# Kernel tuning notes

Hardware: AMD Instinct MI355X
Metric: run time of the kernel (lower is better)

## Reference

```python
import jax, jax.numpy as jnp
import numpy as np

N = 50000          # nodes
E = 600000         # edges
D_IN = 256         # input_feat_dim
H1 = 128           # hidden_dim1
H2 = 64            # hidden_dim2
DK = 64            # trs_depth (total key/value depth)
HEADS = 2


def setup_inputs() -> dict:
    key = jax.random.key(0)
    ks = jax.random.split(key, 12)
    inp = {
        "ns_emb": jax.random.normal(ks[0], (N, D_IN), dtype=jnp.float32),
        "edge_rows": jax.random.randint(ks[1], (E,), 0, N, dtype=jnp.int32),
        "edge_cols": jax.random.randint(ks[2], (E,), 0, N, dtype=jnp.int32),
        "edge_vals": jax.random.uniform(ks[3], (E,), dtype=jnp.float32),
        "condition": jax.random.normal(ks[4], (1, 128, H1), dtype=jnp.float32),
        # GCN linear weights (bias=False), stored [in, out]
        "W_hidden": jax.random.normal(ks[5], (D_IN, H1), dtype=jnp.float32) / np.sqrt(D_IN),
        "W_mu": jax.random.normal(ks[6], (H1, H2), dtype=jnp.float32) / np.sqrt(H1),
        "W_var": jax.random.normal(ks[7], (H1, H2), dtype=jnp.float32) / np.sqrt(H1),
        # MultiHeadAttention (bias-free) projections
        "Wq": jax.random.normal(ks[8], (H1, DK), dtype=jnp.float32) / np.sqrt(H1),
        "Wk": jax.random.normal(ks[9], (H1, DK), dtype=jnp.float32) / np.sqrt(H1),
        "Wv": jax.random.normal(ks[10], (H1, DK), dtype=jnp.float32) / np.sqrt(H1),
        "Wo": jax.random.normal(ks[11], (DK, H1), dtype=jnp.float32) / np.sqrt(DK),
    }
    return inp


def _spmm(rows, cols, vals, x):
    # sparse [N,N] @ x  via gather + segment-sum over COO edges
    gathered = vals[:, None] * x[cols]            # [E, d]
    return jax.ops.segment_sum(gathered, rows, num_segments=N)


def _gcn(x, W, rows, cols, vals):
    # dropout is identity in eval mode
    support = jax.nn.leaky_relu(x @ W)            # [N, out]
    out = _spmm(rows, cols, vals, support)        # [N, out]
    return jax.nn.leaky_relu(out)


def _mha(q, kv, Wq, Wk, Wv, Wo):
    # MoEL-style MultiHeadAttention, bias-free, no mask/dropout
    B, Lq, _ = q.shape
    Lk = kv.shape[1]
    dk = DK // HEADS
    Q = (q @ Wq).reshape(B, Lq, HEADS, dk).transpose(0, 2, 1, 3) * (dk ** -0.5)
    K = (kv @ Wk).reshape(B, Lk, HEADS, dk).transpose(0, 2, 1, 3)
    V = (kv @ Wv).reshape(B, Lk, HEADS, dk).transpose(0, 2, 1, 3)
    logits = jnp.einsum("bhqd,bhkd->bhqk", Q, K)
    w = jax.nn.softmax(logits, axis=-1)
    ctx = jnp.einsum("bhqk,bhkd->bhqd", w, V)
    ctx = ctx.transpose(0, 2, 1, 3).reshape(B, Lq, DK)
    return ctx @ Wo, w


def reference(ns_emb, edge_rows, edge_cols, edge_vals, condition,
              W_hidden, W_mu, W_var, Wq, Wk, Wv, Wo):
    hidden = _gcn(ns_emb, W_hidden, edge_rows, edge_cols, edge_vals)   # [N, H1]
    attended, _ = _mha(hidden[None], condition, Wq, Wk, Wv, Wo)        # [1, N, H1]
    h = attended[0]
    mu = _gcn(h, W_mu, edge_rows, edge_cols, edge_vals)                # [N, H2]
    var = _gcn(h, W_var, edge_rows, edge_cols, edge_vals)              # [N, H2]
    return mu, var
```

## Files before the change

kernel.cpp:

```cpp
#include <hip/hip_runtime.h>
#include <hip/hip_bf16.h>
#include <cstdint>


typedef __attribute__((ext_vector_type(8))) short short8;
typedef __attribute__((ext_vector_type(4))) float f32x4;
typedef __attribute__((ext_vector_type(4))) unsigned short ushort4_t;

__device__ __forceinline__ unsigned short f2bf(float f) {
    unsigned int u = __builtin_bit_cast(unsigned int, f);
    u += 0x7fffu + ((u >> 16) & 1u);
    return (unsigned short)(u >> 16);
}
__device__ __forceinline__ float bf2f(unsigned short v) {
    return __builtin_bit_cast(float, (unsigned int)v << 16);
}


__global__ void hist_kernel(const int* __restrict__ rows, int* __restrict__ cnt, int E) {
    int i = blockIdx.x * blockDim.x + threadIdx.x;
    if (i < E) atomicAdd(&cnt[rows[i]], 1);
}

__global__ void scan1_kernel(const int* __restrict__ cnt, int* __restrict__ excl,
                             int* __restrict__ bsum, int N) {
    __shared__ int sh[256];
    int t = threadIdx.x;
    int i = blockIdx.x * 256 + t;
    int v = (i < N) ? cnt[i] : 0;
    sh[t] = v;
    __syncthreads();
    for (int off = 1; off < 256; off <<= 1) {
        int x = (t >= off) ? sh[t - off] : 0;
        __syncthreads();
        sh[t] += x;
        __syncthreads();
    }
    if (i < N) excl[i] = sh[t] - v;
    if (t == 255) bsum[blockIdx.x] = sh[255];
}

__global__ void scan23_kernel(const int* __restrict__ excl, const int* __restrict__ bsum,
                              int* __restrict__ row_start, int* __restrict__ cursor,
                              int nb, int N, int E) {
    __shared__ int sh[256];
    int t = threadIdx.x;
    int v = (t < nb) ? bsum[t] : 0;
    sh[t] = v;
    __syncthreads();
    for (int off = 1; off < 256; off <<= 1) {
        int x = (t >= off) ? sh[t - off] : 0;
        __syncthreads();
        sh[t] += x;
        __syncthreads();
    }
    int boff = (blockIdx.x > 0) ? sh[blockIdx.x - 1] : 0;
    int i = blockIdx.x * 256 + t;
    if (i < N) {
        int w = excl[i] + boff;
        row_start[i] = w;
        cursor[i] = w;
    }
    if (i == 0) row_start[N] = E;
}

__global__ void scatter_kernel(const int* __restrict__ rows, const int* __restrict__ colsIn,
                               const float* __restrict__ valsIn, int* __restrict__ cursor,
                               int2* __restrict__ pack, int E) {
    int i = blockIdx.x * blockDim.x + threadIdx.x;
    if (i < E) {
        int r = rows[i];
        int p = atomicAdd(&cursor[r], 1);
        pack[p] = make_int2(colsIn[i], __float_as_int(valsIn[i]));
    }
}


__global__ __launch_bounds__(256) void prep_kv_kernel(
    const float* __restrict__ Wh, const float* __restrict__ Wq,
    const float* __restrict__ cond,
    const float* __restrict__ Wk, const float* __restrict__ Wv,
    const float* __restrict__ Wo, const float* __restrict__ Wmu,
    const float* __restrict__ Wvar,
    unsigned short* __restrict__ WhT, unsigned short* __restrict__ WqT,
    unsigned short* __restrict__ Ktt, unsigned short* __restrict__ Vt,
    unsigned short* __restrict__ WomT)
{
    const int t = threadIdx.x;
    const int bid = blockIdx.x;
    if (bid < 160) {
        int idx = bid * 256 + t;
        if (idx < 32768) {
            int n = idx & 127, k = idx >> 7;
            WhT[n * 256 + k] = f2bf(Wh[k * 128 + n]);
        } else {
            int i = idx - 32768, n = i & 63, k = i >> 6;
            WqT[n * 128 + k] = f2bf(Wq[k * 64 + n]);
        }
    } else if (bid < 224) {
        int b2 = bid - 160;
        __shared__ float c[2][128];
        c[t >> 7][t & 127] = cond[b2 * 256 + t];
        __syncthreads();
        int j = b2 * 2 + (t >> 7);
        int tl = t & 127;
        const float* W = (tl < 64) ? Wk : Wv;
        int col = tl & 63;
        float acc = 0.f;
#pragma unroll 8
        for (int k = 0; k < 128; ++k) acc = fmaf(c[t >> 7][k], W[k * 64 + col], acc);
        int h = col >> 5, d = col & 31;
        if (tl < 64) Ktt[((size_t)h * 128 + j) * 32 + d] = f2bf(acc * 0.17677669529663687f);
        else         Vt[((size_t)h * 32 + d) * 128 + j] = f2bf(acc);
    } else {
        int wb = bid - 224;
        __shared__ float WoTl[128 * 65];
#pragma unroll
        for (int i = 0; i < 32; ++i) {
            int idx = t + 256 * i;
            int d = idx >> 7, k = idx & 127;
            WoTl[k * 65 + d] = Wo[idx];
        }
        __syncthreads();
        int o = wb * 256 + t;
        int d = o & 63, n = o >> 6;
        const float* W = (n < 64) ? Wmu : Wvar;
        int j = n & 63;
        float acc = 0.f;
#pragma unroll 8
        for (int k = 0; k < 128; ++k) acc = fmaf(WoTl[k * 65 + d], W[k * 64 + j], acc);
        WomT[n * 64 + d] = f2bf(acc);
    }
}


__global__ __launch_bounds__(256) void gcn1_gemm(
    const float* __restrict__ A, const unsigned short* __restrict__ BT,
    unsigned short* __restrict__ C, int M)
{
    __shared__ unsigned short As[128][72];
    __shared__ unsigned short Bs[128][72];

    const int tid = threadIdx.x;
    const int lane = tid & 63, wave = tid >> 6;
    const int wm = wave & 1, wn = wave >> 1;
    const int quad = lane >> 4, l16 = lane & 15;
    const int r0 = blockIdx.x * 128;

    f32x4 acc[4][4];
#pragma unroll
    for (int mt = 0; mt < 4; ++mt)
#pragma unroll
        for (int nt = 0; nt < 4; ++nt)
#pragma unroll
            for (int r = 0; r < 4; ++r) acc[mt][nt][r] = 0.f;

    for (int kc = 0; kc < 256; kc += 64) {
#pragma unroll
        for (int i = 0; i < 8; ++i) {
            int f = tid + 256 * i;
            int row = f >> 4, kq = (f & 15) << 2;
            int gr = r0 + row;
            if (gr >= M) gr = M - 1;
            float4 v = *reinterpret_cast<const float4*>(&A[(size_t)gr * 256 + kc + kq]);
            unsigned int lo, hi;
            asm("v_cvt_pk_bf16_f32 %0, %1, %2" : "=v"(lo) : "v"(v.x), "v"(v.y));
            asm("v_cvt_pk_bf16_f32 %0, %1, %2" : "=v"(hi) : "v"(v.z), "v"(v.w));
            *reinterpret_cast<uint2*>(&As[row][kq]) = make_uint2(lo, hi);
        }
#pragma unroll
        for (int i = 0; i < 4; ++i) {
            int f = tid + 256 * i;
            int n = f >> 3, k8 = (f & 7) << 3;
            *reinterpret_cast<short8*>(&Bs[n][k8]) =
                *reinterpret_cast<const short8*>(&BT[(size_t)n * 256 + kc + k8]);
        }
        __syncthreads();

#pragma unroll
        for (int ks = 0; ks < 2; ++ks) {
            const int koff = ks * 32 + quad * 8;
            short8 a[4], b[4];
#pragma unroll
            for (int mt = 0; mt < 4; ++mt)
                a[mt] = *reinterpret_cast<const short8*>(&As[wm * 64 + mt * 16 + l16][koff]);
#pragma unroll
            for (int nt = 0; nt < 4; ++nt)
                b[nt] = *reinterpret_cast<const short8*>(&Bs[wn * 64 + nt * 16 + l16][koff]);
#pragma unroll
            for (int mt = 0; mt < 4; ++mt)
#pragma unroll
                for (int nt = 0; nt < 4; ++nt)
                    acc[mt][nt] = __builtin_amdgcn_mfma_f32_16x16x32_bf16(
                        a[mt], b[nt], acc[mt][nt], 0, 0, 0);
        }
        __syncthreads();
    }

#pragma unroll
    for (int mt = 0; mt < 4; ++mt)
#pragma unroll
        for (int nt = 0; nt < 4; ++nt) {
            int gc = wn * 64 + nt * 16 + l16;
#pragma unroll
            for (int r = 0; r < 4; ++r) {
                int gr = r0 + wm * 64 + mt * 16 + quad * 4 + r;
                if (gr < M) {
                    float v = acc[mt][nt][r];
                    v = v > 0.f ? v : 0.01f * v;
                    C[(size_t)gr * 128 + gc] = f2bf(v);
                }
            }
        }
}


__global__ __launch_bounds__(256) void attn_muvar_kernel(
    const unsigned short* __restrict__ support1,
    const int* __restrict__ row_start,
    const int2* __restrict__ pack,
    const unsigned short* __restrict__ WqT,
    const unsigned short* __restrict__ Ktt,
    const unsigned short* __restrict__ Vt,
    const unsigned short* __restrict__ WomT,
    unsigned short* __restrict__ muvar,
    int M)
{
    __shared__ unsigned short Ap[128 * 136];
    __shared__ unsigned short Bp[10240];
    __shared__ unsigned short Cp[128 * 72];
    __shared__ float redm[2][128];
    __shared__ float reds[2][128];

    const int tid = threadIdx.x;
    const int lane = tid & 63, wave = tid >> 6;
    const int wm = wave & 1, wn = wave >> 1;
    const int quad = lane >> 4, l16 = lane & 15;
    const int r0 = blockIdx.x * 128;

#pragma unroll
    for (int i = 0; i < 4; ++i) {
        int f = tid + 256 * i;
        int n = f >> 4, k8 = (f & 15) << 3;
        *reinterpret_cast<short8*>(&Bp[n * 136 + k8]) =
            *reinterpret_cast<const short8*>(&WqT[(size_t)n * 128 + k8]);
    }

    {
        const int fo = lane * 2;
        const int base = r0 + wave * 32;
        const bool fast = (base + 32 <= M);
        int bnds = 0;
        if (fast && lane <= 32) bnds = row_start[base + lane];

        for (int it = 0; it < 32; ++it) {
            int row = wave * 32 + it;
            int s, e;
            if (fast) {
                s = __shfl(bnds, it, 64);
                e = __shfl(bnds, it + 1, 64);
            } else {
                int gr = r0 + row;
                if (gr >= M) gr = M - 1;
                s = __builtin_amdgcn_readfirstlane(row_start[gr]);
                e = __builtin_amdgcn_readfirstlane(row_start[gr + 1]);
            }

            float ax[8], ay[8];
#pragma unroll
            for (int k = 0; k < 8; ++k) { ax[k] = 0.f; ay[k] = 0.f; }

            int i = s;
            for (; i + 8 <= e; i += 8) {
                int2 p[8];
                unsigned int x[8];
#pragma unroll
                for (int k = 0; k < 8; ++k) p[k] = pack[i + k];
#pragma unroll
                for (int k = 0; k < 8; ++k)
                    x[k] = *reinterpret_cast<const unsigned int*>(&support1[(size_t)p[k].x * 128 + fo]);
#pragma unroll
                for (int k = 0; k < 8; ++k) {
                    float v = __int_as_float(p[k].y);
                    ax[k] = fmaf(v, bf2f((unsigned short)x[k]), ax[k]);
                    ay[k] = fmaf(v, bf2f((unsigned short)(x[k] >> 16)), ay[k]);
                }
            }
            if (i < e) {
                int2 p[8];
                unsigned int x[8];
#pragma unroll
                for (int k = 0; k < 8; ++k) {
                    int idx = i + k;
                    p[k] = pack[idx < e ? idx : e - 1];
                }
#pragma unroll
                for (int k = 0; k < 8; ++k)
                    x[k] = *reinterpret_cast<const unsigned int*>(&support1[(size_t)p[k].x * 128 + fo]);
#pragma unroll
                for (int k = 0; k < 8; ++k) {
                    float v = (i + k < e) ? __int_as_float(p[k].y) : 0.f;
                    ax[k] = fmaf(v, bf2f((unsigned short)x[k]), ax[k]);
                    ay[k] = fmaf(v, bf2f((unsigned short)(x[k] >> 16)), ay[k]);
                }
            }

            float ox = ((ax[0] + ax[1]) + (ax[2] + ax[3])) + ((ax[4] + ax[5]) + (ax[6] + ax[7]));
            float oy = ((ay[0] + ay[1]) + (ay[2] + ay[3])) + ((ay[4] + ay[5]) + (ay[6] + ay[7]));
            ox = ox > 0.f ? ox : 0.01f * ox;
            oy = oy > 0.f ? oy : 0.01f * oy;
            unsigned int w = (unsigned int)f2bf(ox) | ((unsigned int)f2bf(oy) << 16);
            *reinterpret_cast<unsigned int*>(&Ap[row * 136 + fo]) = w;
        }
    }
    __syncthreads();

    {
        f32x4 accq[4][2];
#pragma unroll
        for (int mt = 0; mt < 4; ++mt)
#pragma unroll
            for (int nt = 0; nt < 2; ++nt)
#pragma unroll
                for (int r = 0; r < 4; ++r) accq[mt][nt][r] = 0.f;
#pragma unroll
        for (int ks = 0; ks < 4; ++ks) {
            const int koff = ks * 32 + quad * 8;
            short8 a[4], b[2];
#pragma unroll
            for (int mt = 0; mt < 4; ++mt)
                a[mt] = *reinterpret_cast<const short8*>(&Ap[(wm * 64 + mt * 16 + l16) * 136 + koff]);
#pragma unroll
            for (int nt = 0; nt < 2; ++nt)
                b[nt] = *reinterpret_cast<const short8*>(&Bp[(wn * 32 + nt * 16 + l16) * 136 + koff]);
#pragma unroll
            for (int mt = 0; mt < 4; ++mt)
#pragma unroll
                for (int nt = 0; nt < 2; ++nt)
                    accq[mt][nt] = __builtin_amdgcn_mfma_f32_16x16x32_bf16(
                        a[mt], b[nt], accq[mt][nt], 0, 0, 0);
        }
#pragma unroll
        for (int mt = 0; mt < 4; ++mt)
#pragma unroll
            for (int nt = 0; nt < 2; ++nt) {
                int col = wn * 32 + nt * 16 + l16;
#pragma unroll
                for (int r = 0; r < 4; ++r) {
                    int row = wm * 64 + mt * 16 + quad * 4 + r;
                    Cp[row * 72 + col] = f2bf(accq[mt][nt][r]);
                }
            }
    }
    __syncthreads();

    for (int h = 0; h < 2; ++h) {
#pragma unroll
        for (int i = 0; i < 2; ++i) {
            int f = tid + 256 * i;
            int key = f >> 2, d8 = (f & 3) << 3;
            *reinterpret_cast<short8*>(&Bp[key * 40 + d8]) =
                *reinterpret_cast<const short8*>(&Ktt[((size_t)h * 128 + key) * 32 + d8]);
        }
#pragma unroll
        for (int i = 0; i < 2; ++i) {
            int f = tid + 256 * i;
            int d = f >> 4, k8 = (f & 15) << 3;
            *reinterpret_cast<short8*>(&Bp[5120 + d * 136 + k8]) =
                *reinterpret_cast<const short8*>(&Vt[((size_t)h * 32 + d) * 128 + k8]);
        }
        __syncthreads();

        f32x4 accl[4][4];
        {
            short8 a[4], b[4];
#pragma unroll
            for (int mt = 0; mt < 4; ++mt)
                a[mt] = *reinterpret_cast<const short8*>(&Cp[(wm * 64 + mt * 16 + l16) * 72 + h * 32 + quad * 8]);
#pragma unroll
            for (int nt = 0; nt < 4; ++nt)
                b[nt] = *reinterpret_cast<const short8*>(&Bp[(wn * 64 + nt * 16 + l16) * 40 + quad * 8]);
#pragma unroll
            for (int mt = 0; mt < 4; ++mt)
#pragma unroll
                for (int nt = 0; nt < 4; ++nt) {
                    f32x4 z; z[0] = 0.f; z[1] = 0.f; z[2] = 0.f; z[3] = 0.f;
                    accl[mt][nt] = __builtin_amdgcn_mfma_f32_16x16x32_bf16(a[mt], b[nt], z, 0, 0, 0);
                }
        }

#pragma unroll
        for (int mt = 0; mt < 4; ++mt)
#pragma unroll
            for (int r = 0; r < 4; ++r) {
                float mx = fmaxf(fmaxf(accl[mt][0][r], accl[mt][1][r]),
                                 fmaxf(accl[mt][2][r], accl[mt][3][r]));
#pragma unroll
                for (int off = 1; off < 16; off <<= 1)
                    mx = fmaxf(mx, __shfl_xor(mx, off, 64));
                if (l16 == 0) redm[wn][wm * 64 + mt * 16 + quad * 4 + r] = mx;
            }
        __syncthreads();
#pragma unroll
        for (int mt = 0; mt < 4; ++mt)
#pragma unroll
            for (int r = 0; r < 4; ++r) {
                int lr = wm * 64 + mt * 16 + quad * 4 + r;
                float fm = fmaxf(redm[0][lr], redm[1][lr]);
                float s = 0.f;
#pragma unroll
                for (int nt = 0; nt < 4; ++nt) {
                    float e = __expf(accl[mt][nt][r] - fm);
                    accl[mt][nt][r] = e;
                    s += e;
                }
#pragma unroll
                for (int off = 1; off < 16; off <<= 1)
                    s += __shfl_xor(s, off, 64);
                if (l16 == 0) reds[wn][lr] = s;
            }
        __syncthreads();
#pragma unroll
        for (int mt = 0; mt < 4; ++mt)
#pragma unroll
            for (int r = 0; r < 4; ++r) {
                int lr = wm * 64 + mt * 16 + quad * 4 + r;
                float inv = 1.0f / (reds[0][lr] + reds[1][lr]);
#pragma unroll
                for (int nt = 0; nt < 4; ++nt)
                    Ap[lr * 136 + wn * 64 + nt * 16 + l16] = f2bf(accl[mt][nt][r] * inv);
            }
        __syncthreads();

        {
            f32x4 accc[4];
#pragma unroll
            for (int mt = 0; mt < 4; ++mt)
#pragma unroll
                for (int r = 0; r < 4; ++r) accc[mt][r] = 0.f;
#pragma unroll
            for (int ks = 0; ks < 4; ++ks) {
                const int koff = ks * 32 + quad * 8;
                short8 a[4];
#pragma unroll
                for (int mt = 0; mt < 4; ++mt)
                    a[mt] = *reinterpret_cast<const short8*>(&Ap[(wm * 64 + mt * 16 + l16) * 136 + koff]);
                short8 bb = *reinterpret_cast<const short8*>(&Bp[5120 + (wn * 16 + l16) * 136 + koff]);
#pragma unroll
                for (int mt = 0; mt < 4; ++mt)
                    accc[mt] = __builtin_amdgcn_mfma_f32_16x16x32_bf16(a[mt], bb, accc[mt], 0, 0, 0);
            }
#pragma unroll
            for (int mt = 0; mt < 4; ++mt)
#pragma unroll
                for (int r = 0; r < 4; ++r) {
                    int row = wm * 64 + mt * 16 + quad * 4 + r;
                    Cp[row * 72 + h * 32 + wn * 16 + l16] = f2bf(accc[mt][r]);
                }
        }
        __syncthreads();
    }

#pragma unroll
    for (int i = 0; i < 4; ++i) {
        int f = tid + 256 * i;
        int n = f >> 3, k8 = (f & 7) << 3;
        *reinterpret_cast<short8*>(&Bp[n * 72 + k8]) =
            *reinterpret_cast<const short8*>(&WomT[(size_t)n * 64 + k8]);
    }
    __syncthreads();
    {
        f32x4 accf[4][4];
#pragma unroll
        for (int mt = 0; mt < 4; ++mt)
#pragma unroll
            for (int nt = 0; nt < 4; ++nt)
#pragma unroll
                for (int r = 0; r < 4; ++r) accf[mt][nt][r] = 0.f;
#pragma unroll
        for (int ks = 0; ks < 2; ++ks) {
            const int koff = ks * 32 + quad * 8;
            short8 a[4], b[4];
#pragma unroll
            for (int mt = 0; mt < 4; ++mt)
                a[mt] = *reinterpret_cast<const short8*>(&Cp[(wm * 64 + mt * 16 + l16) * 72 + koff]);
#pragma unroll
            for (int nt = 0; nt < 4; ++nt)
                b[nt] = *reinterpret_cast<const short8*>(&Bp[(wn * 64 + nt * 16 + l16) * 72 + koff]);
#pragma unroll
            for (int mt = 0; mt < 4; ++mt)
#pragma unroll
                for (int nt = 0; nt < 4; ++nt)
                    accf[mt][nt] = __builtin_amdgcn_mfma_f32_16x16x32_bf16(
                        a[mt], b[nt], accf[mt][nt], 0, 0, 0);
        }
#pragma unroll
        for (int mt = 0; mt < 4; ++mt)
#pragma unroll
            for (int nt = 0; nt < 4; ++nt) {
                int gc = wn * 64 + nt * 16 + l16;
#pragma unroll
                for (int r = 0; r < 4; ++r) {
                    int gr = r0 + wm * 64 + mt * 16 + quad * 4 + r;
                    if (gr < M) {
                        float v = accf[mt][nt][r];
                        v = v > 0.f ? v : 0.01f * v;
                        muvar[(size_t)gr * 128 + gc] = f2bf(v);
                    }
                }
            }
    }
}


template<bool SPLIT, typename OT>
__global__ __launch_bounds__(256) void spmm_kernel(
    const int* __restrict__ row_start, const int2* __restrict__ pack,
    const unsigned short* __restrict__ X,
    OT* __restrict__ out0, OT* __restrict__ out1, int N)
{
    const int wave = threadIdx.x >> 6, lane = threadIdx.x & 63;
    const int r = blockIdx.x * 4 + wave;
    if (r >= N) return;
    int s = __builtin_amdgcn_readfirstlane(row_start[r]);
    int e = __builtin_amdgcn_readfirstlane(row_start[r + 1]);
    const int fo = lane * 2;

    float ax[8], ay[8];
#pragma unroll
    for (int k = 0; k < 8; ++k) { ax[k] = 0.f; ay[k] = 0.f; }

    int i = s;
    for (; i + 8 <= e; i += 8) {
        int2 p[8];
        unsigned int x[8];
#pragma unroll
        for (int k = 0; k < 8; ++k) p[k] = pack[i + k];
#pragma unroll
        for (int k = 0; k < 8; ++k)
            x[k] = *reinterpret_cast<const unsigned int*>(&X[(size_t)p[k].x * 128 + fo]);
#pragma unroll
        for (int k = 0; k < 8; ++k) {
            float v = __int_as_float(p[k].y);
            ax[k] = fmaf(v, bf2f((unsigned short)x[k]), ax[k]);
            ay[k] = fmaf(v, bf2f((unsigned short)(x[k] >> 16)), ay[k]);
        }
    }
    if (i < e) {
        int2 p[8];
        unsigned int x[8];
#pragma unroll
        for (int k = 0; k < 8; ++k) {
            int idx = i + k;
            p[k] = pack[idx < e ? idx : e - 1];
        }
#pragma unroll
        for (int k = 0; k < 8; ++k)
            x[k] = *reinterpret_cast<const unsigned int*>(&X[(size_t)p[k].x * 128 + fo]);
#pragma unroll
        for (int k = 0; k < 8; ++k) {
            float v = (i + k < e) ? __int_as_float(p[k].y) : 0.f;
            ax[k] = fmaf(v, bf2f((unsigned short)x[k]), ax[k]);
            ay[k] = fmaf(v, bf2f((unsigned short)(x[k] >> 16)), ay[k]);
        }
    }

    float ox = ((ax[0] + ax[1]) + (ax[2] + ax[3])) + ((ax[4] + ax[5]) + (ax[6] + ax[7]));
    float oy = ((ay[0] + ay[1]) + (ay[2] + ay[3])) + ((ay[4] + ay[5]) + (ay[6] + ay[7]));
    ox = ox > 0.f ? ox : 0.01f * ox;
    oy = oy > 0.f ? oy : 0.01f * oy;

    if constexpr (!SPLIT) {
        unsigned int w = (unsigned int)f2bf(ox) | ((unsigned int)f2bf(oy) << 16);
        *reinterpret_cast<unsigned int*>(&out0[(size_t)r * 128 + fo]) = w;
    } else {
        if (lane < 32) {
            *reinterpret_cast<float2*>(&out0[(size_t)r * 64 + fo]) = make_float2(ox, oy);
        } else {
            *reinterpret_cast<float2*>(&out1[(size_t)r * 64 + (fo - 64)]) = make_float2(ox, oy);
        }
    }
}


extern "C" void kernel_launch(void* const* d_in, const int* in_sizes, int n_in,
                              void* d_out, int out_size, void* d_ws, size_t ws_size,
                              hipStream_t stream)
{
    const float* ns_emb   = (const float*)d_in[0];
    const int*   erows    = (const int*)d_in[1];
    const int*   ecols    = (const int*)d_in[2];
    const float* evals    = (const float*)d_in[3];
    const float* cond     = (const float*)d_in[4];
    const float* W_hidden = (const float*)d_in[5];
    const float* W_mu     = (const float*)d_in[6];
    const float* W_var    = (const float*)d_in[7];
    const float* Wq       = (const float*)d_in[8];
    const float* Wk       = (const float*)d_in[9];
    const float* Wv       = (const float*)d_in[10];
    const float* Wo       = (const float*)d_in[11];

    const int N = in_sizes[0] / 256;
    const int E = in_sizes[1];

    typedef unsigned short bf16;
    uint8_t* p = (uint8_t*)d_ws;
    auto alloc = [&](size_t bytes) {
        uint8_t* r = p;
        p += (bytes + 255) & ~(size_t)255;
        return r;
    };
    bf16* support1 = (bf16*)alloc(sizeof(bf16) * (size_t)N * 128);
    bf16* muvarb   = (bf16*)alloc(sizeof(bf16) * (size_t)N * 128);
    bf16* Ktt      = (bf16*)alloc(sizeof(bf16) * 2 * 128 * 32);
    bf16* Vt       = (bf16*)alloc(sizeof(bf16) * 2 * 32 * 128);
    bf16* WhT      = (bf16*)alloc(sizeof(bf16) * 128 * 256);
    bf16* WqT      = (bf16*)alloc(sizeof(bf16) * 64 * 128);
    bf16* WomT     = (bf16*)alloc(sizeof(bf16) * 128 * 64);
    int*  cnt      = (int*)alloc(sizeof(int) * N);
    int*  excl     = (int*)alloc(sizeof(int) * N);
    int*  bsum     = (int*)alloc(sizeof(int) * 256);
    int*  row_start= (int*)alloc(sizeof(int) * (N + 1));
    int*  cursor   = (int*)alloc(sizeof(int) * N);
    int2* pack     = (int2*)alloc(sizeof(int2) * E);

    hipMemsetAsync(cnt, 0, sizeof(int) * N, stream);
    hist_kernel<<<(E + 255) / 256, 256, 0, stream>>>(erows, cnt, E);
    int nb = (N + 255) / 256;
    scan1_kernel<<<nb, 256, 0, stream>>>(cnt, excl, bsum, N);
    scan23_kernel<<<nb, 256, 0, stream>>>(excl, bsum, row_start, cursor, nb, N, E);
    scatter_kernel<<<(E + 255) / 256, 256, 0, stream>>>(erows, ecols, evals, cursor, pack, E);

    prep_kv_kernel<<<256, 256, 0, stream>>>(W_hidden, Wq, cond, Wk, Wv,
                                            Wo, W_mu, W_var,
                                            WhT, WqT, Ktt, Vt, WomT);

    const int mb = (N + 127) / 128;
    const int sblocks = (N + 3) / 4;

    gcn1_gemm<<<mb, 256, 0, stream>>>(ns_emb, WhT, support1, N);

    attn_muvar_kernel<<<mb, 256, 0, stream>>>(support1, row_start, pack,
                                              WqT, Ktt, Vt, WomT, muvarb, N);

    float* out = (float*)d_out;
    spmm_kernel<true, float><<<sblocks, 256, 0, stream>>>(
        row_start, pack, muvarb, out, out + (size_t)N * 64, N);
}
```

Measured before the change: 301.4 us.

## Split first SpMM out of attention kernel and halve attention tile rows

Moves the first-layer sparse aggregation out of the fused attention kernel into a separate wave-per-row spmm_kernel that writes a bf16 hidden buffer. The attention kernel then just loads the dense hidden tile and works on 64-row tiles instead of 128, which cuts LDS use and doubles the block count. The fused version had each wave walk 32 rows one after another with poor parallelism. The split costs an extra kernel launch and a write and read of an N×128 bf16 intermediate.

```diff
diff --git a/kernel.cpp b/kernel.cpp
--- a/kernel.cpp
+++ b/kernel.cpp
@@ -216,9 +216,7 @@
 
 
 __global__ __launch_bounds__(256) void attn_muvar_kernel(
-    const unsigned short* __restrict__ support1,
-    const int* __restrict__ row_start,
-    const int2* __restrict__ pack,
+    const unsigned short* __restrict__ hidden,
     const unsigned short* __restrict__ WqT,
     const unsigned short* __restrict__ Ktt,
     const unsigned short* __restrict__ Vt,
@@ -226,18 +224,27 @@
     unsigned short* __restrict__ muvar,
     int M)
 {
-    __shared__ unsigned short Ap[128 * 136];
+    __shared__ unsigned short Ap[64 * 136];
     __shared__ unsigned short Bp[10240];
-    __shared__ unsigned short Cp[128 * 72];
-    __shared__ float redm[2][128];
-    __shared__ float reds[2][128];
+    __shared__ unsigned short Cp[64 * 72];
+    __shared__ float redm[2][64];
+    __shared__ float reds[2][64];
 
     const int tid = threadIdx.x;
     const int lane = tid & 63, wave = tid >> 6;
     const int wm = wave & 1, wn = wave >> 1;
     const int quad = lane >> 4, l16 = lane & 15;
-    const int r0 = blockIdx.x * 128;
-
+    const int r0 = blockIdx.x * 64;
+
+#pragma unroll
+    for (int i = 0; i < 4; ++i) {
+        int f = tid + 256 * i;
+        int row = f >> 4, k8 = (f & 15) << 3;
+        int gr = r0 + row;
+        if (gr >= M) gr = M - 1;
+        *reinterpret_cast<short8*>(&Ap[row * 136 + k8]) =
+            *reinterpret_cast<const short8*>(&hidden[(size_t)gr * 128 + k8]);
+    }
 #pragma unroll
     for (int i = 0; i < 4; ++i) {
         int f = tid + 256 * i;
@@ -245,80 +252,12 @@
         *reinterpret_cast<short8*>(&Bp[n * 136 + k8]) =
             *reinterpret_cast<const short8*>(&WqT[(size_t)n * 128 + k8]);
     }
+    __syncthreads();
 
     {
-        const int fo = lane * 2;
-        const int base = r0 + wave * 32;
-        const bool fast = (base + 32 <= M);
-        int bnds = 0;
-        if (fast && lane <= 32) bnds = row_start[base + lane];
-
-        for (int it = 0; it < 32; ++it) {
-            int row = wave * 32 + it;
-            int s, e;
-            if (fast) {
-                s = __shfl(bnds, it, 64);
-                e = __shfl(bnds, it + 1, 64);
-            } else {
-                int gr = r0 + row;
-                if (gr >= M) gr = M - 1;
-                s = __builtin_amdgcn_readfirstlane(row_start[gr]);
-                e = __builtin_amdgcn_readfirstlane(row_start[gr + 1]);
-            }
-
-            float ax[8], ay[8];
-#pragma unroll
-            for (int k = 0; k < 8; ++k) { ax[k] = 0.f; ay[k] = 0.f; }
-
-            int i = s;
-            for (; i + 8 <= e; i += 8) {
-                int2 p[8];
-                unsigned int x[8];
-#pragma unroll
-                for (int k = 0; k < 8; ++k) p[k] = pack[i + k];
-#pragma unroll
-                for (int k = 0; k < 8; ++k)
-                    x[k] = *reinterpret_cast<const unsigned int*>(&support1[(size_t)p[k].x * 128 + fo]);
-#pragma unroll
-                for (int k = 0; k < 8; ++k) {
-                    float v = __int_as_float(p[k].y);
-                    ax[k] = fmaf(v, bf2f((unsigned short)x[k]), ax[k]);
-                    ay[k] = fmaf(v, bf2f((unsigned short)(x[k] >> 16)), ay[k]);
-                }
-            }
-            if (i < e) {
-                int2 p[8];
-                unsigned int x[8];
-#pragma unroll
-                for (int k = 0; k < 8; ++k) {
-                    int idx = i + k;
-                    p[k] = pack[idx < e ? idx : e - 1];
-                }
-#pragma unroll
-                for (int k = 0; k < 8; ++k)
-                    x[k] = *reinterpret_cast<const unsigned int*>(&support1[(size_t)p[k].x * 128 + fo]);
-#pragma unroll
-                for (int k = 0; k < 8; ++k) {
-                    float v = (i + k < e) ? __int_as_float(p[k].y) : 0.f;
-                    ax[k] = fmaf(v, bf2f((unsigned short)x[k]), ax[k]);
-                    ay[k] = fmaf(v, bf2f((unsigned short)(x[k] >> 16)), ay[k]);
-                }
-            }
-
-            float ox = ((ax[0] + ax[1]) + (ax[2] + ax[3])) + ((ax[4] + ax[5]) + (ax[6] + ax[7]));
-            float oy = ((ay[0] + ay[1]) + (ay[2] + ay[3])) + ((ay[4] + ay[5]) + (ay[6] + ay[7]));
-            ox = ox > 0.f ? ox : 0.01f * ox;
-            oy = oy > 0.f ? oy : 0.01f * oy;
-            unsigned int w = (unsigned int)f2bf(ox) | ((unsigned int)f2bf(oy) << 16);
-            *reinterpret_cast<unsigned int*>(&Ap[row * 136 + fo]) = w;
-        }
-    }
-    __syncthreads();
-
-    {
-        f32x4 accq[4][2];
-#pragma unroll
-        for (int mt = 0; mt < 4; ++mt)
+        f32x4 accq[2][2];
+#pragma unroll
+        for (int mt = 0; mt < 2; ++mt)
 #pragma unroll
             for (int nt = 0; nt < 2; ++nt)
 #pragma unroll
@@ -326,28 +265,28 @@
 #pragma unroll
         for (int ks = 0; ks < 4; ++ks) {
             const int koff = ks * 32 + quad * 8;
-            short8 a[4], b[2];
-#pragma unroll
-            for (int mt = 0; mt < 4; ++mt)
-                a[mt] = *reinterpret_cast<const short8*>(&Ap[(wm * 64 + mt * 16 + l16) * 136 + koff]);
+            short8 a[2], b[2];
+#pragma unroll
+            for (int mt = 0; mt < 2; ++mt)
+                a[mt] = *reinterpret_cast<const short8*>(&Ap[(wm * 32 + mt * 16 + l16) * 136 + koff]);
 #pragma unroll
             for (int nt = 0; nt < 2; ++nt)
                 b[nt] = *reinterpret_cast<const short8*>(&Bp[(wn * 32 + nt * 16 + l16) * 136 + koff]);
 #pragma unroll
-            for (int mt = 0; mt < 4; ++mt)
+            for (int mt = 0; mt < 2; ++mt)
 #pragma unroll
                 for (int nt = 0; nt < 2; ++nt)
                     accq[mt][nt] = __builtin_amdgcn_mfma_f32_16x16x32_bf16(
                         a[mt], b[nt], accq[mt][nt], 0, 0, 0);
         }
 #pragma unroll
-        for (int mt = 0; mt < 4; ++mt)
+        for (int mt = 0; mt < 2; ++mt)
 #pragma unroll
             for (int nt = 0; nt < 2; ++nt) {
                 int col = wn * 32 + nt * 16 + l16;
 #pragma unroll
                 for (int r = 0; r < 4; ++r) {
-                    int row = wm * 64 + mt * 16 + quad * 4 + r;
+                    int row = wm * 32 + mt * 16 + quad * 4 + r;
                     Cp[row * 72 + col] = f2bf(accq[mt][nt][r]);
                 }
             }
@@ -371,17 +310,17 @@
         }
         __syncthreads();
 
-        f32x4 accl[4][4];
+        f32x4 accl[2][4];
         {
-            short8 a[4], b[4];
-#pragma unroll
-            for (int mt = 0; mt < 4; ++mt)
-                a[mt] = *reinterpret_cast<const short8*>(&Cp[(wm * 64 + mt * 16 + l16) * 72 + h * 32 + quad * 8]);
+            short8 a[2], b[4];
+#pragma unroll
+            for (int mt = 0; mt < 2; ++mt)
+                a[mt] = *reinterpret_cast<const short8*>(&Cp[(wm * 32 + mt * 16 + l16) * 72 + h * 32 + quad * 8]);
 #pragma unroll
             for (int nt = 0; nt < 4; ++nt)
                 b[nt] = *reinterpret_cast<const short8*>(&Bp[(wn * 64 + nt * 16 + l16) * 40 + quad * 8]);
 #pragma unroll
-            for (int mt = 0; mt < 4; ++mt)
+            for (int mt = 0; mt < 2; ++mt)
 #pragma unroll
                 for (int nt = 0; nt < 4; ++nt) {
                     f32x4 z; z[0] = 0.f; z[1] = 0.f; z[2] = 0.f; z[3] = 0.f;
@@ -390,7 +329,7 @@
         }
 
 #pragma unroll
-        for (int mt = 0; mt < 4; ++mt)
+        for (int mt = 0; mt < 2; ++mt)
 #pragma unroll
             for (int r = 0; r < 4; ++r) {
                 float mx = fmaxf(fmaxf(accl[mt][0][r], accl[mt][1][r]),
@@ -398,14 +337,14 @@
 #pragma unroll
                 for (int off = 1; off < 16; off <<= 1)
                     mx = fmaxf(mx, __shfl_xor(mx, off, 64));
-                if (l16 == 0) redm[wn][wm * 64 + mt * 16 + quad * 4 + r] = mx;
-            }
-        __syncthreads();
-#pragma unroll
-        for (int mt = 0; mt < 4; ++mt)
+                if (l16 == 0) redm[wn][wm * 32 + mt * 16 + quad * 4 + r] = mx;
+            }
+        __syncthreads();
+#pragma unroll
+        for (int mt = 0; mt < 2; ++mt)
 #pragma unroll
             for (int r = 0; r < 4; ++r) {
-                int lr = wm * 64 + mt * 16 + quad * 4 + r;
+                int lr = wm * 32 + mt * 16 + quad * 4 + r;
                 float fm = fmaxf(redm[0][lr], redm[1][lr]);
                 float s = 0.f;
 #pragma unroll
@@ -421,10 +360,10 @@
             }
         __syncthreads();
 #pragma unroll
-        for (int mt = 0; mt < 4; ++mt)
+        for (int mt = 0; mt < 2; ++mt)
 #pragma unroll
             for (int r = 0; r < 4; ++r) {
-                int lr = wm * 64 + mt * 16 + quad * 4 + r;
+                int lr = wm * 32 + mt * 16 + quad * 4 + r;
                 float inv = 1.0f / (reds[0][lr] + reds[1][lr]);
 #pragma unroll
                 for (int nt = 0; nt < 4; ++nt)
@@ -433,28 +372,28 @@
         __syncthreads();
 
         {
-            f32x4 accc[4];
-#pragma unroll
-            for (int mt = 0; mt < 4; ++mt)
+            f32x4 accc[2];
+#pragma unroll
+            for (int mt = 0; mt < 2; ++mt)
 #pragma unroll
                 for (int r = 0; r < 4; ++r) accc[mt][r] = 0.f;
 #pragma unroll
             for (int ks = 0; ks < 4; ++ks) {
                 const int koff = ks * 32 + quad * 8;
-                short8 a[4];
-#pragma unroll
-                for (int mt = 0; mt < 4; ++mt)
-                    a[mt] = *reinterpret_cast<const short8*>(&Ap[(wm * 64 + mt * 16 + l16) * 136 + koff]);
+                short8 a[2];
+#pragma unroll
+                for (int mt = 0; mt < 2; ++mt)
+                    a[mt] = *reinterpret_cast<const short8*>(&Ap[(wm * 32 + mt * 16 + l16) * 136 + koff]);
                 short8 bb = *reinterpret_cast<const short8*>(&Bp[5120 + (wn * 16 + l16) * 136 + koff]);
 #pragma unroll
-                for (int mt = 0; mt < 4; ++mt)
+                for (int mt = 0; mt < 2; ++mt)
                     accc[mt] = __builtin_amdgcn_mfma_f32_16x16x32_bf16(a[mt], bb, accc[mt], 0, 0, 0);
             }
 #pragma unroll
-            for (int mt = 0; mt < 4; ++mt)
+            for (int mt = 0; mt < 2; ++mt)
 #pragma unroll
                 for (int r = 0; r < 4; ++r) {
-                    int row = wm * 64 + mt * 16 + quad * 4 + r;
+                    int row = wm * 32 + mt * 16 + quad * 4 + r;
                     Cp[row * 72 + h * 32 + wn * 16 + l16] = f2bf(accc[mt][r]);
                 }
         }
@@ -470,9 +409,9 @@
     }
     __syncthreads();
     {
-        f32x4 accf[4][4];
-#pragma unroll
-        for (int mt = 0; mt < 4; ++mt)
+        f32x4 accf[2][4];
+#pragma unroll
+        for (int mt = 0; mt < 2; ++mt)
 #pragma unroll
             for (int nt = 0; nt < 4; ++nt)
 #pragma unroll
@@ -480,28 +419,28 @@
 #pragma unroll
         for (int ks = 0; ks < 2; ++ks) {
             const int koff = ks * 32 + quad * 8;
-            short8 a[4], b[4];
-#pragma unroll
-            for (int mt = 0; mt < 4; ++mt)
-                a[mt] = *reinterpret_cast<const short8*>(&Cp[(wm * 64 + mt * 16 + l16) * 72 + koff]);
+            short8 a[2], b[4];
+#pragma unroll
+            for (int mt = 0; mt < 2; ++mt)
+                a[mt] = *reinterpret_cast<const short8*>(&Cp[(wm * 32 + mt * 16 + l16) * 72 + koff]);
 #pragma unroll
             for (int nt = 0; nt < 4; ++nt)
                 b[nt] = *reinterpret_cast<const short8*>(&Bp[(wn * 64 + nt * 16 + l16) * 72 + koff]);
 #pragma unroll
-            for (int mt = 0; mt < 4; ++mt)
+            for (int mt = 0; mt < 2; ++mt)
 #pragma unroll
                 for (int nt = 0; nt < 4; ++nt)
                     accf[mt][nt] = __builtin_amdgcn_mfma_f32_16x16x32_bf16(
                         a[mt], b[nt], accf[mt][nt], 0, 0, 0);
         }
 #pragma unroll
-        for (int mt = 0; mt < 4; ++mt)
+        for (int mt = 0; mt < 2; ++mt)
 #pragma unroll
             for (int nt = 0; nt < 4; ++nt) {
                 int gc = wn * 64 + nt * 16 + l16;
 #pragma unroll
                 for (int r = 0; r < 4; ++r) {
-                    int gr = r0 + wm * 64 + mt * 16 + quad * 4 + r;
+                    int gr = r0 + wm * 32 + mt * 16 + quad * 4 + r;
                     if (gr < M) {
                         float v = accf[mt][nt][r];
                         v = v > 0.f ? v : 0.01f * v;
@@ -611,6 +550,7 @@
         return r;
     };
     bf16* support1 = (bf16*)alloc(sizeof(bf16) * (size_t)N * 128);
+    bf16* hidden   = (bf16*)alloc(sizeof(bf16) * (size_t)N * 128);
     bf16* muvarb   = (bf16*)alloc(sizeof(bf16) * (size_t)N * 128);
     bf16* Ktt      = (bf16*)alloc(sizeof(bf16) * 2 * 128 * 32);
     bf16* Vt       = (bf16*)alloc(sizeof(bf16) * 2 * 32 * 128);
@@ -635,13 +575,16 @@
                                             Wo, W_mu, W_var,
                                             WhT, WqT, Ktt, Vt, WomT);
 
-    const int mb = (N + 127) / 128;
+    const int mb128 = (N + 127) / 128;
+    const int mb64  = (N + 63) / 64;
     const int sblocks = (N + 3) / 4;
 
-    gcn1_gemm<<<mb, 256, 0, stream>>>(ns_emb, WhT, support1, N);
-
-    attn_muvar_kernel<<<mb, 256, 0, stream>>>(support1, row_start, pack,
-                                              WqT, Ktt, Vt, WomT, muvarb, N);
+    gcn1_gemm<<<mb128, 256, 0, stream>>>(ns_emb, WhT, support1, N);
+    spmm_kernel<false, bf16><<<sblocks, 256, 0, stream>>>(
+        row_start, pack, support1, hidden, nullptr, N);
+
+    attn_muvar_kernel<<<mb64, 256, 0, stream>>>(hidden, WqT, Ktt, Vt,
+                                                WomT, muvarb, N);
 
     float* out = (float*)d_out;
     spmm_kernel<true, float><<<sblocks, 256, 0, stream>>>(
```

Result: faster. 268.8 us (-10.8%).
